# Kernel optimization log

Hardware: AMD Instinct MI355X
Metric: run time of the kernel (lower is better)

## Reference

```python
import jax, jax.numpy as jnp
import numpy as np

B, S, D, H, E, K = 2, 1024, 512, 2048, 64, 2
EPS = 1e-5


def setup_inputs() -> dict:
    key = jax.random.key(0)
    ks = jax.random.split(key, 5)
    s = 0.02  # small init scale for stability
    return {
        "x": jax.random.normal(ks[0], (B, S, D), dtype=jnp.float32),
        "Wg": jax.random.normal(ks[1], (D, E), dtype=jnp.float32) * s,
        "bg": jnp.zeros((E,), dtype=jnp.float32),
        "W1": jax.random.normal(ks[2], (E, D, H), dtype=jnp.float32) * s,
        "b1": jnp.zeros((E, H), dtype=jnp.float32),
        "W2": jax.random.normal(ks[3], (E, H, D), dtype=jnp.float32) * s,
        "b2": jnp.zeros((E, D), dtype=jnp.float32),
        "gamma": jnp.ones((D,), dtype=jnp.float32),
        "beta": jnp.zeros((D,), dtype=jnp.float32),
    }


def reference(x, Wg, bg, W1, b1, W2, b2, gamma, beta):
    # Gating: softmax over experts, keep top-k weights, zero the rest (scatter)
    probs = jax.nn.softmax(x @ Wg + bg, axis=-1)          # [B,S,E]
    topk_vals, topk_idx = jax.lax.top_k(probs, K)          # [B,S,K]
    sparse_w = jnp.sum(
        jax.nn.one_hot(topk_idx, E, dtype=probs.dtype) * topk_vals[..., None],
        axis=-2,
    )                                                      # [B,S,E]

    # Dense MoE: run every expert FFN on every token (faithful to source)
    h = jax.nn.relu(jnp.einsum('bsd,edh->bseh', x, W1) + b1)   # [B,S,E,H]
    expert_out = jnp.einsum('bseh,ehd->bsed', h, W2) + b2      # [B,S,E,D]

    # Weighted combine + residual
    out = jnp.einsum('bse,bsed->bsd', sparse_w, expert_out) + x

    # LayerNorm (eps=1e-5, elementwise affine)
    mu = out.mean(-1, keepdims=True)
    var = ((out - mu) ** 2).mean(-1, keepdims=True)
    return (out - mu) * jax.lax.rsqrt(var + EPS) * gamma + beta
```

## Files before the change

### kernel.cpp

```cpp
#include <hip/hip_runtime.h>
#include <hip/hip_bf16.h>

#define NTOK 2048
#define DIM 512
#define HID 2048
#define NEXP 64
#define NSLICE 8
#define HSLICE 256
#define TT 64
#define LN_EPS 1e-5f

typedef __bf16 bf16x8 __attribute__((ext_vector_type(8)));
typedef float f32x4 __attribute__((ext_vector_type(4)));

__global__ void init_kernel(float4* __restrict__ accb, int* __restrict__ counts) {
    int i = blockIdx.x * blockDim.x + threadIdx.x;
    accb[i] = make_float4(0.f, 0.f, 0.f, 0.f);
    if (i < NEXP) counts[i] = 0;
}

__global__ void gate_kernel(const float* __restrict__ x,
                            const float* __restrict__ Wg,
                            const float* __restrict__ bg,
                            int* __restrict__ counts,
                            int* __restrict__ btok,
                            float* __restrict__ bw) {
    const int t = blockIdx.x;
    const int lane = threadIdx.x;
    __shared__ float xs[DIM];
    const float4* xrow = (const float4*)(x + (size_t)t * DIM);
    ((float4*)xs)[lane] = xrow[lane];
    ((float4*)xs)[lane + 64] = xrow[lane + 64];
    __syncthreads();

    float acc = bg[lane];
    #pragma unroll 8
    for (int d = 0; d < DIM; d++) acc += xs[d] * Wg[d * NEXP + lane];

    float m = acc;
    #pragma unroll
    for (int off = 32; off; off >>= 1) m = fmaxf(m, __shfl_xor(m, off));
    float p = __expf(acc - m);
    float ssum = p;
    #pragma unroll
    for (int off = 32; off; off >>= 1) ssum += __shfl_xor(ssum, off);
    float prob = p / ssum;

    float v1 = prob; int i1 = lane;
    #pragma unroll
    for (int off = 32; off; off >>= 1) {
        float ov = __shfl_xor(v1, off);
        int   oi = __shfl_xor(i1, off);
        if (ov > v1 || (ov == v1 && oi < i1)) { v1 = ov; i1 = oi; }
    }
    float v2 = (lane == i1) ? -1e30f : prob; int i2 = lane;
    #pragma unroll
    for (int off = 32; off; off >>= 1) {
        float ov = __shfl_xor(v2, off);
        int   oi = __shfl_xor(i2, off);
        if (ov > v2 || (ov == v2 && oi < i2)) { v2 = ov; i2 = oi; }
    }

    if (lane == 0) {
        int s0 = atomicAdd(&counts[i1], 1);
        btok[i1 * NTOK + s0] = t;  bw[i1 * NTOK + s0] = v1;
        int s1 = atomicAdd(&counts[i2], 1);
        btok[i2 * NTOK + s1] = t;  bw[i2 * NTOK + s1] = v2;
    }
}

__global__ __launch_bounds__(256, 2) void ffn_kernel(
    const float* __restrict__ x,
    const float* __restrict__ W1, const float* __restrict__ b1,
    const float* __restrict__ W2, const float* __restrict__ b2,
    const int* __restrict__ counts,
    const int* __restrict__ btok, const float* __restrict__ bw,
    float* __restrict__ accb)
{
    extern __shared__ char smem[];
    const int e = blockIdx.x >> 3;
    const int s = blockIdx.x & 7;
    const int n = counts[e];
    if (n <= 0) return;

    const int tid  = threadIdx.x;
    const int lane = tid & 63;
    const int wid  = tid >> 6;
    const int lq   = lane >> 4;
    const int lm   = lane & 15;

    const float* W1e = W1 + (size_t)e * DIM * HID;
    const float* W2e = W2 + (size_t)e * HID * DIM;
    const int*   btoke = btok + e * NTOK;
    const float* bwe   = bw   + e * NTOK;

    for (int t0 = 0; t0 < n; t0 += TT) {
        const int tiln = min(TT, n - t0);

        f32x4 acc[4][4];
        #pragma unroll
        for (int i = 0; i < 4; i++)
            #pragma unroll
            for (int j = 0; j < 4; j++) acc[i][j] = (f32x4)0.0f;

        for (int kc2 = 0; kc2 < 2; kc2++) {
            const int kbase = kc2 * 256;
            __syncthreads();
            #pragma unroll
            for (int it = 0; it < 8; it++) {
                int ci = it * 256 + tid;
                int tr = ci >> 5;
                int kc = ci & 31;
                char* dst = smem + tr * 512 + ((kc ^ (tr & 7)) * 16);
                if (tr < tiln) {
                    const float* xp = x + (size_t)btoke[t0 + tr] * DIM + kbase + kc * 8;
                    float4 f0 = *(const float4*)(xp);
                    float4 f1 = *(const float4*)(xp + 4);
                    bf16x8 v;
                    v[0]=(__bf16)f0.x; v[1]=(__bf16)f0.y; v[2]=(__bf16)f0.z; v[3]=(__bf16)f0.w;
                    v[4]=(__bf16)f1.x; v[5]=(__bf16)f1.y; v[6]=(__bf16)f1.z; v[7]=(__bf16)f1.w;
                    *(bf16x8*)dst = v;
                } else {
                    bf16x8 z = (bf16x8)0.0f;
                    *(bf16x8*)dst = z;
                }
            }
            __syncthreads();

            for (int ks = 0; ks < 8; ks++) {
                bf16x8 af[4];
                int kcA = ks * 4 + lq;
                #pragma unroll
                for (int mt = 0; mt < 4; mt++) {
                    int tr = mt * 16 + lm;
                    af[mt] = *(const bf16x8*)(smem + tr * 512 + ((kcA ^ (tr & 7)) * 16));
                }
                int kk = kbase + ks * 32 + lq * 8;
                #pragma unroll
                for (int nt = 0; nt < 4; nt++) {
                    int hglob = s * HSLICE + wid * 64 + nt * 16 + lm;
                    const float* wp = W1e + (size_t)kk * HID + hglob;
                    bf16x8 bfv;
                    #pragma unroll
                    for (int j = 0; j < 8; j++) bfv[j] = (__bf16)wp[(size_t)j * HID];
                    #pragma unroll
                    for (int mt = 0; mt < 4; mt++)
                        acc[nt][mt] = __builtin_amdgcn_mfma_f32_16x16x32_bf16(
                            af[mt], bfv, acc[nt][mt], 0, 0, 0);
                }
            }
        }

        #pragma unroll
        for (int nt = 0; nt < 4; nt++) {
            int hloc0 = wid * 64 + nt * 16 + lm;
            float b1v = b1[e * HID + s * HSLICE + hloc0];
            #pragma unroll
            for (int mt = 0; mt < 4; mt++) {
                #pragma unroll
                for (int r = 0; r < 4; r++) {
                    int tr = mt * 16 + lq * 4 + r;
                    float v = fmaxf(acc[nt][mt][r] + b1v, 0.f);
                    *(__bf16*)(smem + 32768 + tr * 512 +
                               (((hloc0 >> 3) ^ (tr & 7)) * 16) + (hloc0 & 7) * 2) = (__bf16)v;
                }
            }
        }
        __syncthreads();

        for (int ch = 0; ch < 2; ch++) {
            f32x4 yacc[4][4];
            #pragma unroll
            for (int i = 0; i < 4; i++)
                #pragma unroll
                for (int j = 0; j < 4; j++) yacc[i][j] = (f32x4)0.0f;

            for (int ks = 0; ks < 8; ks++) {
                bf16x8 af[4];
                int kcA = ks * 4 + lq;
                #pragma unroll
                for (int mt = 0; mt < 4; mt++) {
                    int tr = mt * 16 + lm;
                    af[mt] = *(const bf16x8*)(smem + 32768 + tr * 512 + ((kcA ^ (tr & 7)) * 16));
                }
                int hh = s * HSLICE + ks * 32 + lq * 8;
                #pragma unroll
                for (int nt = 0; nt < 4; nt++) {
                    int d = wid * 128 + ch * 64 + nt * 16 + lm;
                    const float* wp = W2e + (size_t)hh * DIM + d;
                    bf16x8 bfv;
                    #pragma unroll
                    for (int j = 0; j < 8; j++) bfv[j] = (__bf16)wp[(size_t)j * DIM];
                    #pragma unroll
                    for (int mt = 0; mt < 4; mt++)
                        yacc[nt][mt] = __builtin_amdgcn_mfma_f32_16x16x32_bf16(
                            af[mt], bfv, yacc[nt][mt], 0, 0, 0);
                }
            }
            float b2s[4];
            #pragma unroll
            for (int nt = 0; nt < 4; nt++) {
                int d = wid * 128 + ch * 64 + nt * 16 + lm;
                b2s[nt] = (s == 0) ? b2[e * DIM + d] : 0.f;
            }
            #pragma unroll
            for (int mt = 0; mt < 4; mt++) {
                #pragma unroll
                for (int r = 0; r < 4; r++) {
                    int tr = mt * 16 + lq * 4 + r;
                    if (tr < tiln) {
                        int tok = btoke[t0 + tr];
                        float w = bwe[t0 + tr];
                        float* dst = accb + (size_t)tok * DIM;
                        #pragma unroll
                        for (int nt = 0; nt < 4; nt++) {
                            int d = wid * 128 + ch * 64 + nt * 16 + lm;
                            atomicAdd(dst + d, w * (yacc[nt][mt][r] + b2s[nt]));
                        }
                    }
                }
            }
        }
    }
}

__global__ void ln_kernel(const float* __restrict__ x,
                          const float* __restrict__ accb,
                          const float* __restrict__ gamma,
                          const float* __restrict__ beta,
                          float* __restrict__ out) {
    const int t = blockIdx.x;
    const int tid = threadIdx.x;
    __shared__ float red[8];
    const size_t base = (size_t)t * DIM;
    float v0 = x[base + tid] + accb[base + tid];
    float v1 = x[base + 256 + tid] + accb[base + 256 + tid];
    float s  = v0 + v1;
    float sq = v0 * v0 + v1 * v1;
    #pragma unroll
    for (int off = 32; off; off >>= 1) { s += __shfl_xor(s, off); sq += __shfl_xor(sq, off); }
    if ((tid & 63) == 0) { red[tid >> 6] = s; red[4 + (tid >> 6)] = sq; }
    __syncthreads();
    float S  = red[0] + red[1] + red[2] + red[3];
    float SQ = red[4] + red[5] + red[6] + red[7];
    float mu  = S * (1.f / DIM);
    float var = SQ * (1.f / DIM) - mu * mu;
    float inv = rsqrtf(var + LN_EPS);
    out[base + tid]       = (v0 - mu) * inv * gamma[tid]       + beta[tid];
    out[base + 256 + tid] = (v1 - mu) * inv * gamma[256 + tid] + beta[256 + tid];
}

extern "C" void kernel_launch(void* const* d_in, const int* in_sizes, int n_in,
                              void* d_out, int out_size, void* d_ws, size_t ws_size,
                              hipStream_t stream) {
    const float* x     = (const float*)d_in[0];
    const float* Wg    = (const float*)d_in[1];
    const float* bg    = (const float*)d_in[2];
    const float* W1    = (const float*)d_in[3];
    const float* b1    = (const float*)d_in[4];
    const float* W2    = (const float*)d_in[5];
    const float* b2    = (const float*)d_in[6];
    const float* gamma = (const float*)d_in[7];
    const float* beta  = (const float*)d_in[8];

    char* ws = (char*)d_ws;
    int*   counts = (int*)ws;
    int*   btok   = (int*)(ws + 4096);
    float* bwv    = (float*)(ws + 4096 + 524288);
    float* accb   = (float*)(ws + 4096 + 2 * 524288);

    init_kernel<<<1024, 256, 0, stream>>>((float4*)accb, counts);
    gate_kernel<<<NTOK, 64, 0, stream>>>(x, Wg, bg, counts, btok, bwv);
    ffn_kernel<<<NEXP * NSLICE, 256, 65536, stream>>>(x, W1, b1, W2, b2,
                                                      counts, btok, bwv, accb);
    ln_kernel<<<NTOK, 256, 0, stream>>>(x, accb, gamma, beta, (float*)d_out);
}
```

Before: 804.6 us.

## Stage expert weights through LDS as bf16 and load activations directly

Before, each wave gathered W1/W2 elements from global memory with strided scalar loads (eight rows per bf16x8 fragment), so every wave repeated the same loads. The kernel now stages each 32-row weight chunk cooperatively into padded LDS as bf16 with coalesced loads, and waves read MFMA B fragments from LDS. The x tile is no longer staged in LDS; each lane loads its token rows straight into registers. Shared memory shrinks to a static 52 KB and launch bounds rise to 3 blocks per SM, at the cost of two barriers per k-step and no overlap between weight loads and MFMA work.

```diff
diff --git a/kernel.cpp b/kernel.cpp
--- a/kernel.cpp
+++ b/kernel.cpp
@@ -9,6 +9,10 @@
 #define HSLICE 256
 #define TT 64
 #define LN_EPS 1e-5f
+
+#define WS_OFF 0
+#define HS_OFF 20480
+#define SMEM_BYTES 53248
 
 typedef __bf16 bf16x8 __attribute__((ext_vector_type(8)));
 typedef float f32x4 __attribute__((ext_vector_type(4)));
@@ -69,7 +73,25 @@
     }
 }
 
-__global__ __launch_bounds__(256, 2) void ffn_kernel(
+__device__ __forceinline__ void stage_w(const float* __restrict__ src, size_t rs,
+                                        __bf16* __restrict__ wsb, int tid) {
+    #pragma unroll
+    for (int kh = 0; kh < 2; kh++) {
+        float v[16];
+        #pragma unroll
+        for (int u = 0; u < 16; u++)
+            v[u] = src[(size_t)(kh * 16 + u) * rs + tid];
+        #pragma unroll
+        for (int kg = 0; kg < 2; kg++) {
+            bf16x8 pk;
+            #pragma unroll
+            for (int j = 0; j < 8; j++) pk[j] = (__bf16)v[kg * 8 + j];
+            *(bf16x8*)(wsb + tid * 40 + (kh * 2 + kg) * 8) = pk;
+        }
+    }
+}
+
+__global__ __launch_bounds__(256, 3) void ffn_kernel(
     const float* __restrict__ x,
     const float* __restrict__ W1, const float* __restrict__ b1,
     const float* __restrict__ W2, const float* __restrict__ b2,
@@ -77,7 +99,9 @@
     const int* __restrict__ btok, const float* __restrict__ bw,
     float* __restrict__ accb)
 {
-    extern __shared__ char smem[];
+    __shared__ char smem[SMEM_BYTES];
+    __bf16* wsb = (__bf16*)(smem + WS_OFF);
+
     const int e = blockIdx.x >> 3;
     const int s = blockIdx.x & 7;
     const int n = counts[e];
@@ -97,60 +121,52 @@
     for (int t0 = 0; t0 < n; t0 += TT) {
         const int tiln = min(TT, n - t0);
 
+        int  toks[4];
+        bool tv[4];
+        #pragma unroll
+        for (int mt = 0; mt < 4; mt++) {
+            int tr = mt * 16 + lm;
+            tv[mt] = tr < tiln;
+            toks[mt] = tv[mt] ? btoke[t0 + tr] : 0;
+        }
+
         f32x4 acc[4][4];
         #pragma unroll
         for (int i = 0; i < 4; i++)
             #pragma unroll
             for (int j = 0; j < 4; j++) acc[i][j] = (f32x4)0.0f;
 
-        for (int kc2 = 0; kc2 < 2; kc2++) {
-            const int kbase = kc2 * 256;
+        for (int ks = 0; ks < 16; ks++) {
             __syncthreads();
-            #pragma unroll
-            for (int it = 0; it < 8; it++) {
-                int ci = it * 256 + tid;
-                int tr = ci >> 5;
-                int kc = ci & 31;
-                char* dst = smem + tr * 512 + ((kc ^ (tr & 7)) * 16);
-                if (tr < tiln) {
-                    const float* xp = x + (size_t)btoke[t0 + tr] * DIM + kbase + kc * 8;
+            stage_w(W1e + (size_t)(ks * 32) * HID + s * HSLICE, HID, wsb, tid);
+            __syncthreads();
+
+            bf16x8 af[4];
+            #pragma unroll
+            for (int mt = 0; mt < 4; mt++) {
+                if (tv[mt]) {
+                    const float* xp = x + (size_t)toks[mt] * DIM + ks * 32 + lq * 8;
                     float4 f0 = *(const float4*)(xp);
                     float4 f1 = *(const float4*)(xp + 4);
                     bf16x8 v;
                     v[0]=(__bf16)f0.x; v[1]=(__bf16)f0.y; v[2]=(__bf16)f0.z; v[3]=(__bf16)f0.w;
                     v[4]=(__bf16)f1.x; v[5]=(__bf16)f1.y; v[6]=(__bf16)f1.z; v[7]=(__bf16)f1.w;
-                    *(bf16x8*)dst = v;
+                    af[mt] = v;
                 } else {
-                    bf16x8 z = (bf16x8)0.0f;
-                    *(bf16x8*)dst = z;
-                }
-            }
-            __syncthreads();
-
-            for (int ks = 0; ks < 8; ks++) {
-                bf16x8 af[4];
-                int kcA = ks * 4 + lq;
-                #pragma unroll
-                for (int mt = 0; mt < 4; mt++) {
-                    int tr = mt * 16 + lm;
-                    af[mt] = *(const bf16x8*)(smem + tr * 512 + ((kcA ^ (tr & 7)) * 16));
-                }
-                int kk = kbase + ks * 32 + lq * 8;
-                #pragma unroll
-                for (int nt = 0; nt < 4; nt++) {
-                    int hglob = s * HSLICE + wid * 64 + nt * 16 + lm;
-                    const float* wp = W1e + (size_t)kk * HID + hglob;
-                    bf16x8 bfv;
-                    #pragma unroll
-                    for (int j = 0; j < 8; j++) bfv[j] = (__bf16)wp[(size_t)j * HID];
-                    #pragma unroll
-                    for (int mt = 0; mt < 4; mt++)
-                        acc[nt][mt] = __builtin_amdgcn_mfma_f32_16x16x32_bf16(
-                            af[mt], bfv, acc[nt][mt], 0, 0, 0);
-                }
-            }
-        }
-
+                    af[mt] = (bf16x8)0.0f;
+                }
+            }
+            #pragma unroll
+            for (int nt = 0; nt < 4; nt++) {
+                bf16x8 bfv = *(const bf16x8*)(wsb + (wid * 64 + nt * 16 + lm) * 40 + lq * 8);
+                #pragma unroll
+                for (int mt = 0; mt < 4; mt++)
+                    acc[nt][mt] = __builtin_amdgcn_mfma_f32_16x16x32_bf16(
+                        af[mt], bfv, acc[nt][mt], 0, 0, 0);
+            }
+        }
+
+        __syncthreads();
         #pragma unroll
         for (int nt = 0; nt < 4; nt++) {
             int hloc0 = wid * 64 + nt * 16 + lm;
@@ -161,14 +177,13 @@
                 for (int r = 0; r < 4; r++) {
                     int tr = mt * 16 + lq * 4 + r;
                     float v = fmaxf(acc[nt][mt][r] + b1v, 0.f);
-                    *(__bf16*)(smem + 32768 + tr * 512 +
+                    *(__bf16*)(smem + HS_OFF + tr * 512 +
                                (((hloc0 >> 3) ^ (tr & 7)) * 16) + (hloc0 & 7) * 2) = (__bf16)v;
                 }
             }
         }
-        __syncthreads();
-
-        for (int ch = 0; ch < 2; ch++) {
+
+        for (int dh = 0; dh < 2; dh++) {
             f32x4 yacc[4][4];
             #pragma unroll
             for (int i = 0; i < 4; i++)
@@ -176,21 +191,20 @@
                 for (int j = 0; j < 4; j++) yacc[i][j] = (f32x4)0.0f;
 
             for (int ks = 0; ks < 8; ks++) {
+                __syncthreads();
+                stage_w(W2e + (size_t)(s * HSLICE + ks * 32) * DIM + dh * 256, DIM, wsb, tid);
+                __syncthreads();
+
                 bf16x8 af[4];
                 int kcA = ks * 4 + lq;
                 #pragma unroll
                 for (int mt = 0; mt < 4; mt++) {
                     int tr = mt * 16 + lm;
-                    af[mt] = *(const bf16x8*)(smem + 32768 + tr * 512 + ((kcA ^ (tr & 7)) * 16));
-                }
-                int hh = s * HSLICE + ks * 32 + lq * 8;
+                    af[mt] = *(const bf16x8*)(smem + HS_OFF + tr * 512 + ((kcA ^ (tr & 7)) * 16));
+                }
                 #pragma unroll
                 for (int nt = 0; nt < 4; nt++) {
-                    int d = wid * 128 + ch * 64 + nt * 16 + lm;
-                    const float* wp = W2e + (size_t)hh * DIM + d;
-                    bf16x8 bfv;
-                    #pragma unroll
-                    for (int j = 0; j < 8; j++) bfv[j] = (__bf16)wp[(size_t)j * DIM];
+                    bf16x8 bfv = *(const bf16x8*)(wsb + (wid * 64 + nt * 16 + lm) * 40 + lq * 8);
                     #pragma unroll
                     for (int mt = 0; mt < 4; mt++)
                         yacc[nt][mt] = __builtin_amdgcn_mfma_f32_16x16x32_bf16(
@@ -200,7 +214,7 @@
             float b2s[4];
             #pragma unroll
             for (int nt = 0; nt < 4; nt++) {
-                int d = wid * 128 + ch * 64 + nt * 16 + lm;
+                int d = dh * 256 + wid * 64 + nt * 16 + lm;
                 b2s[nt] = (s == 0) ? b2[e * DIM + d] : 0.f;
             }
             #pragma unroll
@@ -214,13 +228,14 @@
                         float* dst = accb + (size_t)tok * DIM;
                         #pragma unroll
                         for (int nt = 0; nt < 4; nt++) {
-                            int d = wid * 128 + ch * 64 + nt * 16 + lm;
+                            int d = dh * 256 + wid * 64 + nt * 16 + lm;
                             atomicAdd(dst + d, w * (yacc[nt][mt][r] + b2s[nt]));
                         }
                     }
                 }
             }
         }
+        __syncthreads();
     }
 }
 
@@ -271,7 +286,7 @@
 
     init_kernel<<<1024, 256, 0, stream>>>((float4*)accb, counts);
     gate_kernel<<<NTOK, 64, 0, stream>>>(x, Wg, bg, counts, btok, bwv);
-    ffn_kernel<<<NEXP * NSLICE, 256, 65536, stream>>>(x, W1, b1, W2, b2,
-                                                      counts, btok, bwv, accb);
+    ffn_kernel<<<NEXP * NSLICE, 256, 0, stream>>>(x, W1, b1, W2, b2,
+                                                  counts, btok, bwv, accb);
     ln_kernel<<<NTOK, 256, 0, stream>>>(x, accb, gamma, beta, (float*)d_out);
 }
```

Measured after the change: 747.0 us. 7.2% less time.
